# Kernel tuning notes

Measured on AMD Instinct MI355X. Metric: run time of the kernel, lower is better.

## Reference

```python
import jax, jax.numpy as jnp
from jax import lax
import numpy as np

L = 8  # db4 filter length
DEC_LO = np.array([-0.010597401784997278, 0.032883011666982945, 0.030841381835986965,
                   -0.18703481171888114, -0.02798376941698385, 0.6308807679295904,
                   0.7148465705525415, 0.23037781330885523], dtype=np.float32)
DEC_HI = np.array([-0.23037781330885523, 0.7148465705525415, -0.6308807679295904,
                   -0.02798376941698385, 0.18703481171888114, 0.030841381835986965,
                   -0.032883011666982945, -0.010597401784997278], dtype=np.float32)
# analysis: correlation kernels are time-reversed decomposition filters (as in pytorch_wavelets)
AF = np.stack([DEC_LO[::-1], DEC_HI[::-1]])  # (2, L)
# synthesis: torch conv_transpose(rec_filt) == lhs-dilated correlation with flip(rec) = dec
SF = np.stack([DEC_LO, DEC_HI])              # (2, L)


def _afb1d(x, axis):
    # analysis filter bank along `axis` of (B, C, H, W); symmetric pad, stride 2
    B, C = x.shape[0], x.shape[1]
    N = x.shape[axis]
    outsize = (N + L - 1) // 2           # pywt symmetric coeff length
    p = 2 * (outsize - 1) - N + L        # total pad
    pad = [(0, 0)] * 4
    pad[axis] = (p // 2, (p + 1) // 2)
    xp = jnp.pad(x, pad, mode='symmetric')
    if axis == 2:
        kern, strides = AF.reshape(2, 1, L, 1), (2, 1)
    else:
        kern, strides = AF.reshape(2, 1, 1, L), (1, 2)
    kern = jnp.asarray(np.tile(kern, (C, 1, 1, 1)), dtype=x.dtype)  # (2C,1,kh,kw)
    return lax.conv_general_dilated(xp, kern, strides, 'VALID',
                                    dimension_numbers=('NCHW', 'OIHW', 'NCHW'),
                                    feature_group_count=C)


def dwt2d(x):
    # single-level 2D db4 DWT, symmetric mode (pytorch_wavelets DWTForward J=1)
    B, C = x.shape[0], x.shape[1]
    lohi = _afb1d(x, 3)                  # (B, 2C, H, W'); ch = c*2 + band_w
    y = _afb1d(lohi, 2)                  # (B, 4C, H', W'); ch = c*4 + band_w*2 + band_h
    y = y.reshape(B, C, 4, y.shape[-2], y.shape[-1])
    return y[:, :, 0], y[:, :, 1:]       # ll (B,C,H',W'), highs (B,C,3,H',W')


def _sfb1d(lo, hi, axis):
    # synthesis filter bank along `axis`: upsample-by-2 transposed conv, crop L-2
    C = lo.shape[1]
    if axis == 2:
        k0, k1 = SF[0].reshape(1, 1, L, 1), SF[1].reshape(1, 1, L, 1)
        dil, pad = (2, 1), [(1, 1), (0, 0)]   # lax pad = (L-1) - (L-2) = 1
    else:
        k0, k1 = SF[0].reshape(1, 1, 1, L), SF[1].reshape(1, 1, 1, L)
        dil, pad = (1, 2), [(0, 0), (1, 1)]
    k0 = jnp.asarray(np.tile(k0, (C, 1, 1, 1)), dtype=lo.dtype)
    k1 = jnp.asarray(np.tile(k1, (C, 1, 1, 1)), dtype=lo.dtype)
    conv = lambda v, k: lax.conv_general_dilated(
        v, k, (1, 1), pad, lhs_dilation=dil,
        dimension_numbers=('NCHW', 'OIHW', 'NCHW'), feature_group_count=C)
    return conv(lo, k0) + conv(hi, k1)


def idwt2d(ll, lh, hl, hh):
    lo = _sfb1d(ll, lh, 2)
    hi = _sfb1d(hl, hh, 2)
    return _sfb1d(lo, hi, 3)


def setup_inputs() -> dict:
    key = jax.random.key(0)
    ks = jax.random.split(key, 5)
    B, Cin, Cout, H, W = 16, 64, 64, 128, 128
    m = (H + L - 1) // 2                 # 67 wavelet modes per axis
    scale = 1.0 / (Cin * Cout)
    x = jax.random.normal(ks[0], (B, Cin, H, W), dtype=jnp.float32)
    ws = {f"w{i + 1}": scale * jax.random.uniform(ks[i + 1], (Cin, Cout, m, m), dtype=jnp.float32)
          for i in range(4)}
    return {"x": x, **ws}


def reference(x, w1, w2, w3, w4):
    ll, highs = dwt2d(x)
    mix = lambda v, w: jnp.einsum('bixy,ioxy->boxy', v, w)  # per-mode channel mixing
    out_ll = mix(ll, w1)
    lh = mix(highs[:, :, 0], w2)
    hl = mix(highs[:, :, 1], w3)
    hh = mix(highs[:, :, 2], w4)
    return idwt2d(out_ll, lh, hl, hh)
```

## Files before the change

kernel.cpp:

```cpp
#include <hip/hip_runtime.h>

#define BB 16
#define CC 64
#define HH 128
#define WW 128
#define MM 67
#define MODES (MM*MM)
#define MC 32
#define NCHUNK 141

typedef float f4 __attribute__((ext_vector_type(4)));

__constant__ float DEC_LO[8] = {-0.010597401784997278f, 0.032883011666982945f, 0.030841381835986965f,
                                -0.18703481171888114f, -0.02798376941698385f, 0.6308807679295904f,
                                0.7148465705525415f, 0.23037781330885523f};
__constant__ float DEC_HI[8] = {-0.23037781330885523f, 0.7148465705525415f, -0.6308807679295904f,
                                -0.02798376941698385f, 0.18703481171888114f, 0.030841381835986965f,
                                -0.032883011666982945f, -0.010597401784997278f};

__global__ __launch_bounds__(256, 2) void dwt_f(const float* __restrict__ x, float* __restrict__ cf) {
    __shared__ float st[2][HH][MM];
    const int bc  = blockIdx.x;
    const int tid = threadIdx.x;
    const float* xr = x + (size_t)bc * HH * WW;

    for (int p = tid; p < HH * MM; p += 256) {
        int wo = p % MM, h = p / MM;
        const float* row = xr + h * WW;
        float lo = 0.f, hi = 0.f;
        int base = 2 * wo - 6;
        #pragma unroll
        for (int k = 0; k < 8; ++k) {
            int i = base + k;
            i = (i < 0) ? (-i - 1) : i;
            i = (i >= WW) ? (2 * WW - 1 - i) : i;
            float v = row[i];
            lo += v * DEC_LO[7 - k];
            hi += v * DEC_HI[7 - k];
        }
        st[0][h][wo] = lo;
        st[1][h][wo] = hi;
    }
    __syncthreads();

    const int NH2 = (MM + 1) / 2;
    float* cfo = cf + (size_t)bc * 4 * MODES;
    for (int q = tid; q < NH2 * MM; q += 256) {
        int wo = q % MM, hp = q / MM;
        int ho0 = 2 * hp, ho1 = 2 * hp + 1;
        #pragma unroll
        for (int fw = 0; fw < 2; ++fw) {
            float rv[10];
            #pragma unroll
            for (int k = 0; k < 10; ++k) {
                int i = 4 * hp - 6 + k;
                i = (i < 0) ? (-i - 1) : i;
                i = (i >= HH) ? (2 * HH - 1 - i) : i;
                rv[k] = st[fw][i][wo];
            }
            float lo0 = 0.f, hi0 = 0.f, lo1 = 0.f, hi1 = 0.f;
            #pragma unroll
            for (int k = 0; k < 8; ++k) {
                lo0 += rv[k]     * DEC_LO[7 - k];
                hi0 += rv[k]     * DEC_HI[7 - k];
                lo1 += rv[k + 2] * DEC_LO[7 - k];
                hi1 += rv[k + 2] * DEC_HI[7 - k];
            }
            float* b0 = cfo + (size_t)(fw * 2 + 0) * MODES;
            float* b1 = cfo + (size_t)(fw * 2 + 1) * MODES;
            b0[ho0 * MM + wo] = lo0;
            b1[ho0 * MM + wo] = hi0;
            if (ho1 < MM) {
                b0[ho1 * MM + wo] = lo1;
                b1[ho1 * MM + wo] = hi1;
            }
        }
    }
}

__global__ __launch_bounds__(256) void mix_k(const float* __restrict__ cf,
                                             const float* __restrict__ w1,
                                             const float* __restrict__ w2,
                                             const float* __restrict__ w3,
                                             const float* __restrict__ w4,
                                             float* __restrict__ out) {
    __shared__ float sc[BB][CC][MC];
    int flat = blockIdx.y * NCHUNK + blockIdx.x;
    {
        const int q = 564 / 8, r = 564 % 8;
        int xcd = flat & 7, j = flat >> 3;
        flat = (xcd < r ? xcd * (q + 1) : r * (q + 1) + (xcd - r) * q) + j;
    }
    const int band = flat / NCHUNK;
    const int m0   = min((flat % NCHUNK) * MC, MODES - MC);
    const int tid  = threadIdx.x;
    const float* w = (band == 0) ? w1 : (band == 1) ? w2 : (band == 2) ? w3 : w4;

    {
        const int c = tid & 7, r0 = tid >> 3;
        #pragma unroll
        for (int p = 0; p < 32; ++p) {
            int r = r0 + (p << 5);
            f4 v = *(const f4*)(cf + ((size_t)(r * 4) + band) * MODES + m0 + c * 4);
            *(f4*)&sc[r >> 6][r & 63][c * 4] = v;
        }
    }
    __syncthreads();

    const int lane = tid & 63, wv = tid >> 6;
    const int o2 = wv * 8 + (lane >> 3);
    const int mc4 = (lane & 7) * 4;
    const size_t IST = (size_t)CC * MODES;
    const float* wpl = w + (size_t)o2 * MODES + m0 + mc4;
    const float* wph = wpl + (size_t)32 * MODES;

    f4 accL[16], accH[16];
    #pragma unroll
    for (int b = 0; b < 16; ++b) { accL[b] = (f4)(0.f); accH[b] = (f4)(0.f); }

    f4 al0, al1, al2, al3, ah0, ah1, ah2, ah3;
    f4 bl0, bl1, bl2, bl3, bh0, bh1, bh2, bh3;
    al0 = *(const f4*)(wpl + 0 * IST);  ah0 = *(const f4*)(wph + 0 * IST);
    al1 = *(const f4*)(wpl + 1 * IST);  ah1 = *(const f4*)(wph + 1 * IST);
    al2 = *(const f4*)(wpl + 2 * IST);  ah2 = *(const f4*)(wph + 2 * IST);
    al3 = *(const f4*)(wpl + 3 * IST);  ah3 = *(const f4*)(wph + 3 * IST);

    #pragma unroll 1
    for (int ib = 0; ib < 64; ib += 8) {
        bl0 = *(const f4*)(wpl + (size_t)(ib + 4) * IST);  bh0 = *(const f4*)(wph + (size_t)(ib + 4) * IST);
        bl1 = *(const f4*)(wpl + (size_t)(ib + 5) * IST);  bh1 = *(const f4*)(wph + (size_t)(ib + 5) * IST);
        bl2 = *(const f4*)(wpl + (size_t)(ib + 6) * IST);  bh2 = *(const f4*)(wph + (size_t)(ib + 6) * IST);
        bl3 = *(const f4*)(wpl + (size_t)(ib + 7) * IST);  bh3 = *(const f4*)(wph + (size_t)(ib + 7) * IST);
        #pragma unroll
        for (int b = 0; b < 16; ++b) {
            f4 s = *(const f4*)&sc[b][ib + 0][mc4];
            accL[b] += s * al0;  accH[b] += s * ah0;
        }
        #pragma unroll
        for (int b = 0; b < 16; ++b) {
            f4 s = *(const f4*)&sc[b][ib + 1][mc4];
            accL[b] += s * al1;  accH[b] += s * ah1;
        }
        #pragma unroll
        for (int b = 0; b < 16; ++b) {
            f4 s = *(const f4*)&sc[b][ib + 2][mc4];
            accL[b] += s * al2;  accH[b] += s * ah2;
        }
        #pragma unroll
        for (int b = 0; b < 16; ++b) {
            f4 s = *(const f4*)&sc[b][ib + 3][mc4];
            accL[b] += s * al3;  accH[b] += s * ah3;
        }
        if (ib + 8 < 64) {
            al0 = *(const f4*)(wpl + (size_t)(ib + 8)  * IST);  ah0 = *(const f4*)(wph + (size_t)(ib + 8)  * IST);
            al1 = *(const f4*)(wpl + (size_t)(ib + 9)  * IST);  ah1 = *(const f4*)(wph + (size_t)(ib + 9)  * IST);
            al2 = *(const f4*)(wpl + (size_t)(ib + 10) * IST);  ah2 = *(const f4*)(wph + (size_t)(ib + 10) * IST);
            al3 = *(const f4*)(wpl + (size_t)(ib + 11) * IST);  ah3 = *(const f4*)(wph + (size_t)(ib + 11) * IST);
        }
        #pragma unroll
        for (int b = 0; b < 16; ++b) {
            f4 s = *(const f4*)&sc[b][ib + 4][mc4];
            accL[b] += s * bl0;  accH[b] += s * bh0;
        }
        #pragma unroll
        for (int b = 0; b < 16; ++b) {
            f4 s = *(const f4*)&sc[b][ib + 5][mc4];
            accL[b] += s * bl1;  accH[b] += s * bh1;
        }
        #pragma unroll
        for (int b = 0; b < 16; ++b) {
            f4 s = *(const f4*)&sc[b][ib + 6][mc4];
            accL[b] += s * bl2;  accH[b] += s * bh2;
        }
        #pragma unroll
        for (int b = 0; b < 16; ++b) {
            f4 s = *(const f4*)&sc[b][ib + 7][mc4];
            accL[b] += s * bl3;  accH[b] += s * bh3;
        }
    }

    #pragma unroll
    for (int b = 0; b < 16; ++b) {
        *(f4*)&out[((size_t)((b * CC + o2) * 4) + band) * MODES + m0 + mc4] = accL[b];
        *(f4*)&out[((size_t)((b * CC + o2 + 32) * 4) + band) * MODES + m0 + mc4] = accH[b];
    }
}

__global__ __launch_bounds__(256, 2) void idwt_f(const float* __restrict__ mx, float* __restrict__ out) {
    __shared__ float su[2][HH][MM];
    const int bc  = blockIdx.x;
    const int tid = threadIdx.x;
    const float* mxb = mx + (size_t)bc * 4 * MODES;

    for (int p = tid; p < 2 * (HH / 2) * MM; p += 256) {
        int wo = p % MM;
        int a  = (p / MM) % (HH / 2);
        int fw = p / (MM * (HH / 2));
        const float* lo = mxb + (size_t)(fw * 2) * MODES + wo;
        const float* hi = lo + MODES;
        float l[4], h4[4];
        #pragma unroll
        for (int q = 0; q < 4; ++q) {
            l[q]  = lo[(a + q) * MM];
            h4[q] = hi[(a + q) * MM];
        }
        float o0 = 0.f, o1 = 0.f;
        #pragma unroll
        for (int q = 0; q < 4; ++q) {
            o0 += l[q] * DEC_LO[2 * q + 1] + h4[q] * DEC_HI[2 * q + 1];
            o1 += l[q] * DEC_LO[2 * q]     + h4[q] * DEC_HI[2 * q];
        }
        su[fw][2 * a][wo]     = o0;
        su[fw][2 * a + 1][wo] = o1;
    }
    __syncthreads();

    float* ob = out + (size_t)bc * HH * WW;
    for (int p = tid; p < HH * (WW / 2); p += 256) {
        int a = p & 63, h = p >> 6;
        float l[4], h4[4];
        #pragma unroll
        for (int q = 0; q < 4; ++q) {
            l[q]  = su[0][h][a + q];
            h4[q] = su[1][h][a + q];
        }
        float o0 = 0.f, o1 = 0.f;
        #pragma unroll
        for (int q = 0; q < 4; ++q) {
            o0 += l[q] * DEC_LO[2 * q + 1] + h4[q] * DEC_HI[2 * q + 1];
            o1 += l[q] * DEC_LO[2 * q]     + h4[q] * DEC_HI[2 * q];
        }
        *(float2*)&ob[h * WW + 2 * a] = make_float2(o0, o1);
    }
}

extern "C" void kernel_launch(void* const* d_in, const int* in_sizes, int n_in,
                              void* d_out, int out_size, void* d_ws, size_t ws_size,
                              hipStream_t stream) {
    const float* x  = (const float*)d_in[0];
    const float* w1 = (const float*)d_in[1];
    const float* w2 = (const float*)d_in[2];
    const float* w3 = (const float*)d_in[3];
    const float* w4 = (const float*)d_in[4];
    float* out = (float*)d_out;

    const size_t COEFF_FLTS = (size_t)BB * CC * 4 * MODES;
    float* buf1 = (float*)d_ws;
    float* buf2 = buf1 + COEFF_FLTS;

    dwt_f<<<BB * CC, 256, 0, stream>>>(x, buf1);
    {
        dim3 grid(NCHUNK, 4);
        mix_k<<<grid, 256, 0, stream>>>(buf1, w1, w2, w3, w4, buf2);
    }
    idwt_f<<<BB * CC, 256, 0, stream>>>(buf2, out);
}
```

Baseline: 233.1 us.

## Split mix kernel batch across two blocks for higher occupancy

The channel-mixing kernel now gives each block 8 batches instead of 16. This halves the shared-memory tile and the accumulator registers, which allows two blocks per CU under the new launch bounds, and doubles the grid to 1136 blocks. The block index mapping is also changed so that the two batch halves of one mode chunk are scheduled close together, which aims to reuse each weight chunk through L2 across the pair. The cost is that every weight tile is now read twice, once per batch half, and a few padded blocks exit early.

```diff
diff --git a/kernel.cpp b/kernel.cpp
--- a/kernel.cpp
+++ b/kernel.cpp
@@ -78,31 +78,32 @@
     }
 }
 
-__global__ __launch_bounds__(256) void mix_k(const float* __restrict__ cf,
-                                             const float* __restrict__ w1,
-                                             const float* __restrict__ w2,
-                                             const float* __restrict__ w3,
-                                             const float* __restrict__ w4,
-                                             float* __restrict__ out) {
-    __shared__ float sc[BB][CC][MC];
-    int flat = blockIdx.y * NCHUNK + blockIdx.x;
-    {
-        const int q = 564 / 8, r = 564 % 8;
-        int xcd = flat & 7, j = flat >> 3;
-        flat = (xcd < r ? xcd * (q + 1) : r * (q + 1) + (xcd - r) * q) + j;
-    }
-    const int band = flat / NCHUNK;
-    const int m0   = min((flat % NCHUNK) * MC, MODES - MC);
+__global__ __launch_bounds__(256, 2) void mix_k(const float* __restrict__ cf,
+                                                const float* __restrict__ w1,
+                                                const float* __restrict__ w2,
+                                                const float* __restrict__ w3,
+                                                const float* __restrict__ w4,
+                                                float* __restrict__ out) {
+    __shared__ float sc[8][CC][MC];
+    const int d   = blockIdx.x;
+    const int cyc = d >> 4, r = d & 15;
+    const int g   = cyc * 8 + (r & 7);
+    const int bh  = r >> 3;
+    if (g >= 4 * NCHUNK) return;
+    const int band = g / NCHUNK;
+    const int m0   = min((g % NCHUNK) * MC, MODES - MC);
     const int tid  = threadIdx.x;
+    const int bg0  = bh * 8;
     const float* w = (band == 0) ? w1 : (band == 1) ? w2 : (band == 2) ? w3 : w4;
 
     {
         const int c = tid & 7, r0 = tid >> 3;
         #pragma unroll
-        for (int p = 0; p < 32; ++p) {
-            int r = r0 + (p << 5);
-            f4 v = *(const f4*)(cf + ((size_t)(r * 4) + band) * MODES + m0 + c * 4);
-            *(f4*)&sc[r >> 6][r & 63][c * 4] = v;
+        for (int p = 0; p < 16; ++p) {
+            int rr = r0 + (p << 5);
+            int b = bg0 + (rr >> 6), i = rr & 63;
+            f4 v = *(const f4*)(cf + ((size_t)((b * CC + i) * 4) + band) * MODES + m0 + c * 4);
+            *(f4*)&sc[rr >> 6][i][c * 4] = v;
         }
     }
     __syncthreads();
@@ -114,9 +115,9 @@
     const float* wpl = w + (size_t)o2 * MODES + m0 + mc4;
     const float* wph = wpl + (size_t)32 * MODES;
 
-    f4 accL[16], accH[16];
+    f4 accL[8], accH[8];
     #pragma unroll
-    for (int b = 0; b < 16; ++b) { accL[b] = (f4)(0.f); accH[b] = (f4)(0.f); }
+    for (int b = 0; b < 8; ++b) { accL[b] = (f4)(0.f); accH[b] = (f4)(0.f); }
 
     f4 al0, al1, al2, al3, ah0, ah1, ah2, ah3;
     f4 bl0, bl1, bl2, bl3, bh0, bh1, bh2, bh3;
@@ -132,22 +133,22 @@
         bl2 = *(const f4*)(wpl + (size_t)(ib + 6) * IST);  bh2 = *(const f4*)(wph + (size_t)(ib + 6) * IST);
         bl3 = *(const f4*)(wpl + (size_t)(ib + 7) * IST);  bh3 = *(const f4*)(wph + (size_t)(ib + 7) * IST);
         #pragma unroll
-        for (int b = 0; b < 16; ++b) {
+        for (int b = 0; b < 8; ++b) {
             f4 s = *(const f4*)&sc[b][ib + 0][mc4];
             accL[b] += s * al0;  accH[b] += s * ah0;
         }
         #pragma unroll
-        for (int b = 0; b < 16; ++b) {
+        for (int b = 0; b < 8; ++b) {
             f4 s = *(const f4*)&sc[b][ib + 1][mc4];
             accL[b] += s * al1;  accH[b] += s * ah1;
         }
         #pragma unroll
-        for (int b = 0; b < 16; ++b) {
+        for (int b = 0; b < 8; ++b) {
             f4 s = *(const f4*)&sc[b][ib + 2][mc4];
             accL[b] += s * al2;  accH[b] += s * ah2;
         }
         #pragma unroll
-        for (int b = 0; b < 16; ++b) {
+        for (int b = 0; b < 8; ++b) {
             f4 s = *(const f4*)&sc[b][ib + 3][mc4];
             accL[b] += s * al3;  accH[b] += s * ah3;
         }
@@ -158,31 +159,31 @@
             al3 = *(const f4*)(wpl + (size_t)(ib + 11) * IST);  ah3 = *(const f4*)(wph + (size_t)(ib + 11) * IST);
         }
         #pragma unroll
-        for (int b = 0; b < 16; ++b) {
+        for (int b = 0; b < 8; ++b) {
             f4 s = *(const f4*)&sc[b][ib + 4][mc4];
             accL[b] += s * bl0;  accH[b] += s * bh0;
         }
         #pragma unroll
-        for (int b = 0; b < 16; ++b) {
+        for (int b = 0; b < 8; ++b) {
             f4 s = *(const f4*)&sc[b][ib + 5][mc4];
             accL[b] += s * bl1;  accH[b] += s * bh1;
         }
         #pragma unroll
-        for (int b = 0; b < 16; ++b) {
+        for (int b = 0; b < 8; ++b) {
             f4 s = *(const f4*)&sc[b][ib + 6][mc4];
             accL[b] += s * bl2;  accH[b] += s * bh2;
         }
         #pragma unroll
-        for (int b = 0; b < 16; ++b) {
+        for (int b = 0; b < 8; ++b) {
             f4 s = *(const f4*)&sc[b][ib + 7][mc4];
             accL[b] += s * bl3;  accH[b] += s * bh3;
         }
     }
 
     #pragma unroll
-    for (int b = 0; b < 16; ++b) {
-        *(f4*)&out[((size_t)((b * CC + o2) * 4) + band) * MODES + m0 + mc4] = accL[b];
-        *(f4*)&out[((size_t)((b * CC + o2 + 32) * 4) + band) * MODES + m0 + mc4] = accH[b];
+    for (int b = 0; b < 8; ++b) {
+        *(f4*)&out[((size_t)(((bg0 + b) * CC + o2) * 4) + band) * MODES + m0 + mc4] = accL[b];
+        *(f4*)&out[((size_t)(((bg0 + b) * CC + o2 + 32) * 4) + band) * MODES + m0 + mc4] = accH[b];
     }
 }
 
@@ -249,9 +250,6 @@
     float* buf2 = buf1 + COEFF_FLTS;
 
     dwt_f<<<BB * CC, 256, 0, stream>>>(x, buf1);
-    {
-        dim3 grid(NCHUNK, 4);
-        mix_k<<<grid, 256, 0, stream>>>(buf1, w1, w2, w3, w4, buf2);
-    }
+    mix_k<<<1136, 256, 0, stream>>>(buf1, w1, w2, w3, w4, buf2);
     idwt_f<<<BB * CC, 256, 0, stream>>>(buf2, out);
 }
```

Result: slower. 262.0 us (+12.4%).

## Stream mix weights into LDS ring buffer with direct global-to-LDS loads

Applied to the files above, without the earlier changes.

In the channel-mixing kernel, weight fetches no longer go through register double-buffers. Each wave now issues global_load_lds transfers into a 4-slot LDS ring. Explicit vmcnt waits keep the loads four input channels ahead of the FMA loop, and the loop is restructured to one input channel per iteration with a hand-written tail. The aim is to cut VGPR pressure and keep more weight traffic in flight, hiding weight-read latency. The trade-offs are about 32KB of extra LDS, a hard occupancy bound of 1, and reliance on manual waitcnt accounting that could hide ordering hazards.

```diff
diff --git a/kernel.cpp b/kernel.cpp
--- a/kernel.cpp
+++ b/kernel.cpp
@@ -10,6 +10,9 @@
 #define NCHUNK 141
 
 typedef float f4 __attribute__((ext_vector_type(4)));
+
+#define AS1 __attribute__((address_space(1)))
+#define AS3 __attribute__((address_space(3)))
 
 __constant__ float DEC_LO[8] = {-0.010597401784997278f, 0.032883011666982945f, 0.030841381835986965f,
                                 -0.18703481171888114f, -0.02798376941698385f, 0.6308807679295904f,
@@ -78,13 +81,14 @@
     }
 }
 
-__global__ __launch_bounds__(256) void mix_k(const float* __restrict__ cf,
-                                             const float* __restrict__ w1,
-                                             const float* __restrict__ w2,
-                                             const float* __restrict__ w3,
-                                             const float* __restrict__ w4,
-                                             float* __restrict__ out) {
+__global__ __launch_bounds__(256, 1) void mix_k(const float* __restrict__ cf,
+                                                const float* __restrict__ w1,
+                                                const float* __restrict__ w2,
+                                                const float* __restrict__ w3,
+                                                const float* __restrict__ w4,
+                                                float* __restrict__ out) {
     __shared__ float sc[BB][CC][MC];
+    __shared__ float swr[4][4][16][MC];
     int flat = blockIdx.y * NCHUNK + blockIdx.x;
     {
         const int q = 564 / 8, r = 564 % 8;
@@ -94,7 +98,28 @@
     const int band = flat / NCHUNK;
     const int m0   = min((flat % NCHUNK) * MC, MODES - MC);
     const int tid  = threadIdx.x;
+    const int lane = tid & 63, wv = tid >> 6;
     const float* w = (band == 0) ? w1 : (band == 1) ? w2 : (band == 2) ? w3 : w4;
+
+    const int  ob0  = wv * 8;
+    const size_t IST = (size_t)CC * MODES;
+    const float* wbase = w + ((size_t)ob0 + (lane >> 5)) * MODES + m0 + (lane & 31);
+
+    #define STAGE(slot, ii)                                                          \
+    {                                                                                \
+        const float* _s = wbase + (size_t)(ii) * IST;                                \
+        _Pragma("unroll")                                                            \
+        for (int _j = 0; _j < 8; ++_j) {                                             \
+            __builtin_amdgcn_global_load_lds(                                        \
+                (const AS1 void*)(_s + (size_t)(2 * _j + ((_j >= 4) ? 24 : 0)) * MODES), \
+                (AS3 void*)&swr[wv][slot][2 * _j][0], 4, 0, 0);                      \
+        }                                                                            \
+    }
+
+    STAGE(0, 0)
+    STAGE(1, 1)
+    STAGE(2, 2)
+    STAGE(3, 3)
 
     {
         const int c = tid & 7, r0 = tid >> 3;
@@ -107,82 +132,52 @@
     }
     __syncthreads();
 
-    const int lane = tid & 63, wv = tid >> 6;
-    const int o2 = wv * 8 + (lane >> 3);
-    const int mc4 = (lane & 7) * 4;
-    const size_t IST = (size_t)CC * MODES;
-    const float* wpl = w + (size_t)o2 * MODES + m0 + mc4;
-    const float* wph = wpl + (size_t)32 * MODES;
+    const int osub = lane >> 3;
+    const int m4q  = (lane & 7) * 4;
+    const int o2   = ob0 + osub;
 
     f4 accL[16], accH[16];
     #pragma unroll
     for (int b = 0; b < 16; ++b) { accL[b] = (f4)(0.f); accH[b] = (f4)(0.f); }
 
-    f4 al0, al1, al2, al3, ah0, ah1, ah2, ah3;
-    f4 bl0, bl1, bl2, bl3, bh0, bh1, bh2, bh3;
-    al0 = *(const f4*)(wpl + 0 * IST);  ah0 = *(const f4*)(wph + 0 * IST);
-    al1 = *(const f4*)(wpl + 1 * IST);  ah1 = *(const f4*)(wph + 1 * IST);
-    al2 = *(const f4*)(wpl + 2 * IST);  ah2 = *(const f4*)(wph + 2 * IST);
-    al3 = *(const f4*)(wpl + 3 * IST);  ah3 = *(const f4*)(wph + 3 * IST);
-
     #pragma unroll 1
-    for (int ib = 0; ib < 64; ib += 8) {
-        bl0 = *(const f4*)(wpl + (size_t)(ib + 4) * IST);  bh0 = *(const f4*)(wph + (size_t)(ib + 4) * IST);
-        bl1 = *(const f4*)(wpl + (size_t)(ib + 5) * IST);  bh1 = *(const f4*)(wph + (size_t)(ib + 5) * IST);
-        bl2 = *(const f4*)(wpl + (size_t)(ib + 6) * IST);  bh2 = *(const f4*)(wph + (size_t)(ib + 6) * IST);
-        bl3 = *(const f4*)(wpl + (size_t)(ib + 7) * IST);  bh3 = *(const f4*)(wph + (size_t)(ib + 7) * IST);
+    for (int i = 0; i < 60; ++i) {
+        asm volatile("s_waitcnt vmcnt(24)" ::: "memory");
+        const int s = i & 3;
+        f4 wl = *(const f4*)&swr[wv][s][osub][m4q];
+        f4 wh = *(const f4*)&swr[wv][s][8 + osub][m4q];
+        STAGE((i + 4) & 3, i + 4)
         #pragma unroll
         for (int b = 0; b < 16; ++b) {
-            f4 s = *(const f4*)&sc[b][ib + 0][mc4];
-            accL[b] += s * al0;  accH[b] += s * ah0;
-        }
-        #pragma unroll
-        for (int b = 0; b < 16; ++b) {
-            f4 s = *(const f4*)&sc[b][ib + 1][mc4];
-            accL[b] += s * al1;  accH[b] += s * ah1;
-        }
-        #pragma unroll
-        for (int b = 0; b < 16; ++b) {
-            f4 s = *(const f4*)&sc[b][ib + 2][mc4];
-            accL[b] += s * al2;  accH[b] += s * ah2;
-        }
-        #pragma unroll
-        for (int b = 0; b < 16; ++b) {
-            f4 s = *(const f4*)&sc[b][ib + 3][mc4];
-            accL[b] += s * al3;  accH[b] += s * ah3;
-        }
-        if (ib + 8 < 64) {
-            al0 = *(const f4*)(wpl + (size_t)(ib + 8)  * IST);  ah0 = *(const f4*)(wph + (size_t)(ib + 8)  * IST);
-            al1 = *(const f4*)(wpl + (size_t)(ib + 9)  * IST);  ah1 = *(const f4*)(wph + (size_t)(ib + 9)  * IST);
-            al2 = *(const f4*)(wpl + (size_t)(ib + 10) * IST);  ah2 = *(const f4*)(wph + (size_t)(ib + 10) * IST);
-            al3 = *(const f4*)(wpl + (size_t)(ib + 11) * IST);  ah3 = *(const f4*)(wph + (size_t)(ib + 11) * IST);
-        }
-        #pragma unroll
-        for (int b = 0; b < 16; ++b) {
-            f4 s = *(const f4*)&sc[b][ib + 4][mc4];
-            accL[b] += s * bl0;  accH[b] += s * bh0;
-        }
-        #pragma unroll
-        for (int b = 0; b < 16; ++b) {
-            f4 s = *(const f4*)&sc[b][ib + 5][mc4];
-            accL[b] += s * bl1;  accH[b] += s * bh1;
-        }
-        #pragma unroll
-        for (int b = 0; b < 16; ++b) {
-            f4 s = *(const f4*)&sc[b][ib + 6][mc4];
-            accL[b] += s * bl2;  accH[b] += s * bh2;
-        }
-        #pragma unroll
-        for (int b = 0; b < 16; ++b) {
-            f4 s = *(const f4*)&sc[b][ib + 7][mc4];
-            accL[b] += s * bl3;  accH[b] += s * bh3;
-        }
-    }
+            f4 sv = *(const f4*)&sc[b][i][m4q];
+            accL[b] += sv * wl;
+            accH[b] += sv * wh;
+        }
+    }
+    #define TAIL(ii, CNT)                                                   \
+    {                                                                       \
+        asm volatile("s_waitcnt vmcnt(" CNT ")" ::: "memory");              \
+        const int s = (ii) & 3;                                             \
+        f4 wl = *(const f4*)&swr[wv][s][osub][m4q];                         \
+        f4 wh = *(const f4*)&swr[wv][s][8 + osub][m4q];                     \
+        _Pragma("unroll")                                                   \
+        for (int b = 0; b < 16; ++b) {                                      \
+            f4 sv = *(const f4*)&sc[b][ii][m4q];                            \
+            accL[b] += sv * wl;                                             \
+            accH[b] += sv * wh;                                             \
+        }                                                                   \
+    }
+    TAIL(60, "24")
+    TAIL(61, "16")
+    TAIL(62, "8")
+    TAIL(63, "0")
+    #undef TAIL
+    #undef STAGE
 
     #pragma unroll
     for (int b = 0; b < 16; ++b) {
-        *(f4*)&out[((size_t)((b * CC + o2) * 4) + band) * MODES + m0 + mc4] = accL[b];
-        *(f4*)&out[((size_t)((b * CC + o2 + 32) * 4) + band) * MODES + m0 + mc4] = accH[b];
+        *(f4*)&out[((size_t)((b * CC + o2) * 4) + band) * MODES + m0 + m4q] = accL[b];
+        *(f4*)&out[((size_t)((b * CC + o2 + 32) * 4) + band) * MODES + m0 + m4q] = accH[b];
     }
 }
 
```

After: 279.4 us. +19.9%, slower.
